# Kernel tuning notes

Hardware: AMD Instinct MI355X
Metric: run time of the kernel (lower is better)

## Reference

```python
import jax, jax.numpy as jnp
import numpy as np
import math

D_MODEL = 1024
N_HEADS = 16
D_HEAD = D_MODEL // N_HEADS

def setup_inputs() -> dict:
    key = jax.random.key(0)
    k1, k2, k3 = jax.random.split(key, 3)
    x = jax.random.normal(k1, (4, 2048, D_MODEL), dtype=jnp.float32)
    # torch Linear weights are [out, in]; kept in that layout, applied as x @ W.T
    s = 1.0 / math.sqrt(D_MODEL)
    W_qkv = jax.random.uniform(k2, (3 * D_MODEL, D_MODEL), jnp.float32, -s, s)
    W_proj = jax.random.uniform(k3, (D_MODEL, D_MODEL), jnp.float32, -s, s)
    return {"x": x, "W_qkv": W_qkv, "W_proj": W_proj}

def reference(x, W_qkv, W_proj):
    B, T, d = x.shape
    qkv = x @ W_qkv.T  # [B,T,3d]
    q, k, v = jnp.split(qkv, 3, axis=-1)
    def split(t):
        return t.reshape(B, T, N_HEADS, D_HEAD).transpose(0, 2, 1, 3)  # [B,H,T,Dh]
    q, k, v = split(q), split(k), split(v)
    scores = jnp.einsum('bhqd,bhkd->bhqk', q, k) / math.sqrt(D_HEAD)
    mask = jnp.tril(jnp.ones((T, T), dtype=bool))
    scores = jnp.where(mask, scores, -jnp.inf)
    attn = jax.nn.softmax(scores, axis=-1)
    out = jnp.einsum('bhqk,bhkd->bhqd', attn, v)  # [B,H,T,Dh]
    out = out.transpose(0, 2, 1, 3).reshape(B, T, d)
    return out @ W_proj.T
```

## Files before the change

kernel.cpp:

```cpp
#include <hip/hip_runtime.h>
#include <hip/hip_bf16.h>
#include <math.h>

typedef __attribute__((ext_vector_type(8))) short short8;
typedef __attribute__((ext_vector_type(4))) float f32x4;
typedef __attribute__((ext_vector_type(16))) float f32x16;
typedef __attribute__((ext_vector_type(2))) unsigned uint2v;
typedef __attribute__((ext_vector_type(4))) unsigned uint4v;

#define B_  4
#define T_  2048
#define DM  1024
#define NH  16
#define DH  64
#define BH  (B_*NH)
#define M_  (B_*T_)

#define QSCALE 0.18033688011112042f

static __device__ __forceinline__ short f2bf(float f) {
  unsigned u = __float_as_uint(f);
  unsigned r = (u + 0x7fff + ((u >> 16) & 1)) >> 16;
  return (short)r;
}

static __device__ __forceinline__ unsigned cvtpk(float lo, float hi) {
  unsigned r;
  asm("v_cvt_pk_bf16_f32 %0, %1, %2" : "=v"(r) : "v"(lo), "v"(hi));
  return r;
}

static __device__ __forceinline__ float expasm(float x) {
  float r;
  asm("v_exp_f32 %0, %1" : "=v"(r) : "v"(x));
  return r;
}

static __device__ __forceinline__ void gload_lds16(const void* g, void* l) {
  __builtin_amdgcn_global_load_lds((const __attribute__((address_space(1))) void*)g,
                                   (__attribute__((address_space(3))) void*)l, 16, 0, 0);
}

__global__ void k_cvt3(const float4* __restrict__ x, const float4* __restrict__ wq,
                       const float4* __restrict__ wp, ushort4* __restrict__ ox,
                       ushort4* __restrict__ oq, ushort4* __restrict__ op) {
  const int n1 = M_ * DM / 4, n2 = 3 * DM * DM / 4, n3 = DM * DM / 4;
  int i = blockIdx.x * 256 + threadIdx.x;
  const float4* src;
  ushort4* dst;
  int j = i;
  if (i < n1) { src = x; dst = ox; }
  else if (i < n1 + n2) { src = wq; dst = oq; j = i - n1; }
  else if (i < n1 + n2 + n3) { src = wp; dst = op; j = i - n1 - n2; }
  else return;
  float4 v = src[j];
  ushort4 o;
  o.x = (ushort)f2bf(v.x); o.y = (ushort)f2bf(v.y);
  o.z = (ushort)f2bf(v.z); o.w = (ushort)f2bf(v.w);
  dst[j] = o;
}

#define GEMM_STAGE(SRCA, SRCB, dA, dB, m0_, n0_, k0_)                          \
  {                                                                            \
    _Pragma("unroll")                                                          \
    for (int i = 0; i < 4; ++i) {                                              \
      int lin = i * 256 + tid;                                                 \
      int row = lin >> 3, pseg = lin & 7;                                      \
      int gseg = pseg ^ (row & 7);                                             \
      gload_lds16(&SRCA[(size_t)((m0_) + row) * DM + (k0_) + gseg * 8],        \
                  &(dA)[lin * 8]);                                             \
    }                                                                          \
    _Pragma("unroll")                                                          \
    for (int i = 0; i < 4; ++i) {                                              \
      int lin = i * 256 + tid;                                                 \
      int row = lin >> 3, pseg = lin & 7;                                      \
      int gseg = pseg ^ (row & 7);                                             \
      gload_lds16(&SRCB[(size_t)((n0_) + row) * DM + (k0_) + gseg * 8],        \
                  &(dB)[lin * 8]);                                             \
    }                                                                          \
  }

#define GEMM_COMPUTE(pA, pB)                                                   \
  {                                                                            \
    _Pragma("unroll")                                                          \
    for (int kk = 0; kk < 2; ++kk) {                                           \
      short8 aF[4], bF[4];                                                     \
      _Pragma("unroll")                                                        \
      for (int m = 0; m < 4; ++m)                                              \
        aF[m] = *(const short8*)&(pA)[(wr * 64 + m * 16 + fr) * 64 +           \
                                      (((kk * 4 + fq) ^ (fr & 7)) * 8)];       \
      _Pragma("unroll")                                                        \
      for (int n = 0; n < 4; ++n)                                              \
        bF[n] = *(const short8*)&(pB)[(wc * 64 + n * 16 + fr) * 64 +           \
                                      (((kk * 4 + fq) ^ (fr & 7)) * 8)];       \
      __builtin_amdgcn_s_setprio(1);                                           \
      _Pragma("unroll")                                                        \
      for (int m = 0; m < 4; ++m)                                              \
        _Pragma("unroll")                                                      \
        for (int n = 0; n < 4; ++n)                                            \
          acc[m][n] = __builtin_amdgcn_mfma_f32_16x16x32_bf16(aF[m], bF[n],    \
                                                              acc[m][n], 0, 0, 0); \
      __builtin_amdgcn_s_setprio(0);                                           \
    }                                                                          \
  }

#define GEMM_KLOOP(SRCA, SRCB, m0_, n0_)                                       \
  GEMM_STAGE(SRCA, SRCB, sA0, sB0, m0_, n0_, 0);                               \
  {                                                                            \
    _Pragma("unroll 1")                                                        \
    for (int t = 0; t < 16; ++t) {                                             \
      short* pA = (t & 1) ? sA1 : sA0;                                         \
      short* pB = (t & 1) ? sB1 : sB0;                                         \
      if (t < 15) {                                                            \
        short* nA = (t & 1) ? sA0 : sA1;                                       \
        short* nB = (t & 1) ? sB0 : sB1;                                       \
        GEMM_STAGE(SRCA, SRCB, nA, nB, m0_, n0_, (t + 1) * 64);                \
        asm volatile("s_waitcnt vmcnt(8)" ::: "memory");                       \
      } else {                                                                 \
        asm volatile("s_waitcnt vmcnt(0)" ::: "memory");                       \
      }                                                                        \
      __builtin_amdgcn_s_barrier();                                            \
      __builtin_amdgcn_sched_barrier(0);                                       \
      GEMM_COMPUTE(pA, pB);                                                    \
      asm volatile("" ::: "memory");                                           \
      __builtin_amdgcn_s_barrier();                                            \
    }                                                                          \
  }

__global__ __launch_bounds__(256, 2) void k_gemm_qkv(
    const short* __restrict__ A,
    const short* __restrict__ W,
    short* __restrict__ Qb, short* __restrict__ Kb, short* __restrict__ Vtb) {
  const int tid = threadIdx.x;
  const int w = tid >> 6, l = tid & 63;
  const int wr = w >> 1, wc = w & 1;
  const int fq = l >> 4, fr = l & 15;
  const int m0 = blockIdx.x * 128;
  const int n0 = blockIdx.y * 128;

  __shared__ short lds[32768];
  short* sA0 = lds;
  short* sA1 = lds + 8192;
  short* sB0 = lds + 16384;
  short* sB1 = lds + 24576;

  f32x4 acc[4][4] = {};
  GEMM_KLOOP(A, W, m0, n0);
  __syncthreads();

  short* sE = lds;
  const int part = n0 >> 10;
  const int b = m0 >> 11, tloc = m0 & 2047;

  if (part < 2) {
    const float sc = part ? 1.0f : QSCALE;
#pragma unroll
    for (int m = 0; m < 4; ++m)
#pragma unroll
      for (int n = 0; n < 4; ++n)
#pragma unroll
        for (int j = 0; j < 4; ++j)
          sE[(wr * 64 + m * 16 + fq * 4 + j) * 136 + wc * 64 + n * 16 + fr] =
              f2bf(acc[m][n][j] * sc);
    __syncthreads();
    short* dst = part ? Kb : Qb;
    const int h0 = (n0 & 1023) >> 6;
#pragma unroll
    for (int v = 0; v < 8; ++v) {
      int vid = v * 256 + tid;
      int row = vid >> 4, seg = vid & 15;
      short8 val = *(const short8*)&sE[row * 136 + seg * 8];
      int h = h0 + (seg >> 3), dh0 = (seg & 7) * 8;
      *(short8*)&dst[(((size_t)(b * NH + h) * T_ + tloc + row)) * DH + dh0] = val;
    }
  } else {
#pragma unroll
    for (int m = 0; m < 4; ++m)
#pragma unroll
      for (int n = 0; n < 4; ++n) {
        uint2v pk;
        pk[0] = cvtpk(acc[m][n][0], acc[m][n][1]);
        pk[1] = cvtpk(acc[m][n][2], acc[m][n][3]);
        *(uint2v*)&sE[(wc * 64 + n * 16 + fr) * 136 + wr * 64 + m * 16 + fq * 4] = pk;
      }
    __syncthreads();
    const int h0 = (n0 & 1023) >> 6;
#pragma unroll
    for (int v = 0; v < 8; ++v) {
      int vid = v * 256 + tid;
      int col = vid >> 4, seg = vid & 15;
      short8 val = *(const short8*)&sE[col * 136 + seg * 8];
      int h = h0 + (col >> 6), dh = col & 63;
      *(short8*)&Vtb[(((size_t)(b * NH + h) * DH + dh)) * T_ + tloc + seg * 8] = val;
    }
  }
}

__global__ __launch_bounds__(256, 2) void k_gemm_proj(
    const short* __restrict__ A,
    const short* __restrict__ W,
    float* __restrict__ C) {
  const int tid = threadIdx.x;
  const int w = tid >> 6, l = tid & 63;
  const int wr = w >> 1, wc = w & 1;
  const int fq = l >> 4, fr = l & 15;
  const int m0 = blockIdx.x * 128;
  const int n0 = blockIdx.y * 128;

  __shared__ short lds[32768];
  short* sA0 = lds;
  short* sA1 = lds + 8192;
  short* sB0 = lds + 16384;
  short* sB1 = lds + 24576;

  f32x4 acc[4][4] = {};
  GEMM_KLOOP(A, W, m0, n0);

#pragma unroll
  for (int m = 0; m < 4; ++m) {
    int row0 = m0 + wr * 64 + m * 16 + fq * 4;
#pragma unroll
    for (int n = 0; n < 4; ++n) {
      int col = n0 + wc * 64 + n * 16 + fr;
#pragma unroll
      for (int j = 0; j < 4; ++j)
        C[(size_t)(row0 + j) * DM + col] = acc[m][n][j];
    }
  }
}

__global__ __launch_bounds__(256, 2) void k_attn7(
    const short* __restrict__ Qb,
    const short* __restrict__ Kb,
    const short* __restrict__ Vtb,
    short* __restrict__ Ob) {
  const int tid = threadIdx.x;
  const int w = tid >> 6, l = tid & 63;
  const int lq = l & 31, hi = l >> 5;
  const int id = blockIdx.x;
  const int u = id >> 6;
  const int bh = id & 63;
  const int qt = (u < 4) ? (7 - u) : (u - 4);
  const int b = bh >> 4, h = bh & 15;

  __shared__ short lds[16384];
  short* sK = lds;
  short* sVt = lds + 8192;

  auto STAGE = [&](int buf, int kt) {
#pragma unroll
    for (int i = 0; i < 2; ++i) {
      int lin = i * 256 + tid;
      int row = lin >> 3, pseg = lin & 7;
      int gseg = pseg ^ (row & 7);
      gload_lds16(&Kb[((size_t)bh * T_ + kt * 64 + row) * DH + gseg * 8],
                  &sK[buf * 4096 + lin * 8]);
    }
#pragma unroll
    for (int i = 0; i < 2; ++i) {
      int lin = i * 256 + tid;
      int row = lin >> 3, pseg = lin & 7;
      int gseg = pseg ^ (row & 7);
      gload_lds16(&Vtb[((size_t)bh * DH + row) * T_ + kt * 64 + gseg * 8],
                  &sVt[buf * 4096 + lin * 8]);
    }
  };

  const int nkt = 4 * qt + 4;
  const int q00 = qt * 256 + w * 32;
  const int q01 = q00 + 128;

  short8 qf0[4], qf1[4];
#pragma unroll
  for (int c = 0; c < 4; ++c) {
    qf0[c] = *(const short8*)&Qb[((size_t)bh * T_ + q00 + lq) * DH + c * 16 + hi * 8];
    qf1[c] = *(const short8*)&Qb[((size_t)bh * T_ + q01 + lq) * DH + c * 16 + hi * 8];
  }
  asm volatile("s_waitcnt vmcnt(0)" ::: "memory");

  float ls0 = 0.f, ls1 = 0.f;
  f32x16 oa0[2] = {}, oa1[2] = {};

  auto CSUB = [&](int kt, const int koff, const short8 (&qf)[4],
                  f32x16 (&oacc)[2], float& lsum, int q0s) {
    f32x16 a0 = {}, a1 = {};
    __builtin_amdgcn_s_setprio(1);
#pragma unroll
    for (int c = 0; c < 4; ++c) {
      short8 kf0 = *(const short8*)&sK[koff + (lq) * 64 + (((2 * c + hi) ^ (lq & 7)) * 8)];
      short8 kf1 = *(const short8*)&sK[koff + (32 + lq) * 64 + (((2 * c + hi) ^ (lq & 7)) * 8)];
      a0 = __builtin_amdgcn_mfma_f32_32x32x16_bf16(kf0, qf[c], a0, 0, 0, 0);
      a1 = __builtin_amdgcn_mfma_f32_32x32x16_bf16(kf1, qf[c], a1, 0, 0, 0);
    }
    __builtin_amdgcn_s_setprio(0);

    if (kt * 64 + 63 > q0s) {
      const int qg = q0s + lq;
#pragma unroll
      for (int r = 0; r < 16; ++r) {
        int kg0 = kt * 64 + (r & 3) + 8 * (r >> 2) + 4 * hi;
        if (kg0 > qg) a0[r] = -1e30f;
        if (kg0 + 32 > qg) a1[r] = -1e30f;
      }
    }

#pragma unroll
    for (int r = 0; r < 16; ++r) {
      a0[r] = expasm(a0[r]);
      a1[r] = expasm(a1[r]);
    }
    {
      float t[8];
#pragma unroll
      for (int i = 0; i < 8; ++i)
        t[i] = (a0[2 * i] + a0[2 * i + 1]) + (a1[2 * i] + a1[2 * i + 1]);
      float u0 = (t[0] + t[1]) + (t[2] + t[3]);
      float u1 = (t[4] + t[5]) + (t[6] + t[7]);
      lsum += u0 + u1;
    }

    short8 pb[4];
#pragma unroll
    for (int st = 0; st < 2; ++st) {
      const f32x16& P = st ? a1 : a0;
      unsigned x0 = cvtpk(P[0], P[1]);
      unsigned x1 = cvtpk(P[2], P[3]);
      unsigned y0 = cvtpk(P[4], P[5]);
      unsigned y1 = cvtpk(P[6], P[7]);
      uint2v r0 = __builtin_amdgcn_permlane32_swap(x0, y0, false, false);
      uint2v r1 = __builtin_amdgcn_permlane32_swap(x1, y1, false, false);
      unsigned x2 = cvtpk(P[8], P[9]);
      unsigned x3 = cvtpk(P[10], P[11]);
      unsigned y2 = cvtpk(P[12], P[13]);
      unsigned y3 = cvtpk(P[14], P[15]);
      uint2v r2 = __builtin_amdgcn_permlane32_swap(x2, y2, false, false);
      uint2v r3 = __builtin_amdgcn_permlane32_swap(x3, y3, false, false);
      uint4v ta, tb;
      ta[0] = r0[0]; ta[1] = r1[0]; ta[2] = r0[1]; ta[3] = r1[1];
      tb[0] = r2[0]; tb[1] = r3[0]; tb[2] = r2[1]; tb[3] = r3[1];
      pb[st * 2 + 0] = __builtin_bit_cast(short8, ta);
      pb[st * 2 + 1] = __builtin_bit_cast(short8, tb);
    }

    __builtin_amdgcn_s_setprio(1);
#pragma unroll
    for (int dt = 0; dt < 2; ++dt) {
#pragma unroll
      for (int c = 0; c < 4; ++c) {
        short8 vf = *(const short8*)&sVt[koff + (dt * 32 + lq) * 64 +
                                         (((2 * c + hi) ^ (lq & 7)) * 8)];
        oacc[dt] = __builtin_amdgcn_mfma_f32_32x32x16_bf16(vf, pb[c], oacc[dt], 0, 0, 0);
      }
    }
    __builtin_amdgcn_s_setprio(0);
  };

  STAGE(0, 0);
  int t = 0;
  while (true) {
    if (t + 1 < nkt) {
      STAGE(1, t + 1);
      asm volatile("s_waitcnt vmcnt(4)" ::: "memory");
    } else {
      asm volatile("s_waitcnt vmcnt(0)" ::: "memory");
    }
    __builtin_amdgcn_s_barrier();
    __builtin_amdgcn_sched_barrier(0);
    if (t * 64 <= q00 + 31) CSUB(t, 0, qf0, oa0, ls0, q00);
    if (t * 64 <= q01 + 31) CSUB(t, 0, qf1, oa1, ls1, q01);
    __builtin_amdgcn_s_barrier();
    if (++t == nkt) break;

    if (t + 1 < nkt) {
      STAGE(0, t + 1);
      asm volatile("s_waitcnt vmcnt(4)" ::: "memory");
    } else {
      asm volatile("s_waitcnt vmcnt(0)" ::: "memory");
    }
    __builtin_amdgcn_s_barrier();
    __builtin_amdgcn_sched_barrier(0);
    if (t * 64 <= q00 + 31) CSUB(t, 4096, qf0, oa0, ls0, q00);
    if (t * 64 <= q01 + 31) CSUB(t, 4096, qf1, oa1, ls1, q01);
    __builtin_amdgcn_s_barrier();
    if (++t == nkt) break;
  }

  ls0 += __shfl_xor(ls0, 32);
  ls1 += __shfl_xor(ls1, 32);
  __syncthreads();
  short* sO = lds + w * 2304;
  const int qr = l >> 1, hf = l & 1;

  {
    float inv = 1.0f / ls0;
#pragma unroll
    for (int dt = 0; dt < 2; ++dt)
#pragma unroll
      for (int r = 0; r < 16; r += 2) {
        int dl = dt * 32 + (r & 3) + 8 * (r >> 2) + 4 * hi;
        *(unsigned*)&sO[lq * 72 + dl] = cvtpk(oa0[dt][r] * inv, oa0[dt][r + 1] * inv);
      }
    asm volatile("s_waitcnt lgkmcnt(0)" ::: "memory");
    __builtin_amdgcn_sched_barrier(0);
    const int tg = q00 - w * 32 + w * 32 + qr;
#pragma unroll
    for (int ss = 0; ss < 4; ++ss) {
      short8 v = *(const short8*)&sO[qr * 72 + hf * 32 + ss * 8];
      *(short8*)&Ob[((size_t)(b * T_) + tg) * DM + h * 64 + hf * 32 + ss * 8] = v;
    }
    asm volatile("s_waitcnt lgkmcnt(0)" ::: "memory");
    __builtin_amdgcn_sched_barrier(0);
  }
  {
    float inv = 1.0f / ls1;
#pragma unroll
    for (int dt = 0; dt < 2; ++dt)
#pragma unroll
      for (int r = 0; r < 16; r += 2) {
        int dl = dt * 32 + (r & 3) + 8 * (r >> 2) + 4 * hi;
        *(unsigned*)&sO[lq * 72 + dl] = cvtpk(oa1[dt][r] * inv, oa1[dt][r + 1] * inv);
      }
    asm volatile("s_waitcnt lgkmcnt(0)" ::: "memory");
    __builtin_amdgcn_sched_barrier(0);
    const int tg = q01 - w * 32 + w * 32 + qr;
#pragma unroll
    for (int ss = 0; ss < 4; ++ss) {
      short8 v = *(const short8*)&sO[qr * 72 + hf * 32 + ss * 8];
      *(short8*)&Ob[((size_t)(b * T_) + tg) * DM + h * 64 + hf * 32 + ss * 8] = v;
    }
  }
}

extern "C" void kernel_launch(void* const* d_in, const int* in_sizes, int n_in,
                              void* d_out, int out_size, void* d_ws, size_t ws_size,
                              hipStream_t stream) {
  const float* x     = (const float*)d_in[0];
  const float* Wqkv  = (const float*)d_in[1];
  const float* Wproj = (const float*)d_in[2];
  float* out = (float*)d_out;

  short* ws = (short*)d_ws;
  short* xbf   = ws;
  short* wqkvb = xbf + (size_t)M_ * DM;
  short* wprjb = wqkvb + (size_t)3 * DM * DM;
  short* Qb    = wprjb + (size_t)DM * DM;
  short* Kb    = Qb + (size_t)BH * T_ * DH;
  short* Vtb   = Kb + (size_t)BH * T_ * DH;
  short* Ob    = Vtb + (size_t)BH * T_ * DH;

  const int ncv = (M_ * DM + 3 * DM * DM + DM * DM) / 4;
  k_cvt3<<<(ncv + 255) / 256, 256, 0, stream>>>(
      (const float4*)x, (const float4*)Wqkv, (const float4*)Wproj,
      (ushort4*)xbf, (ushort4*)wqkvb, (ushort4*)wprjb);

  k_gemm_qkv<<<dim3(M_ / 128, 3 * DM / 128), 256, 0, stream>>>(xbf, wqkvb, Qb, Kb, Vtb);
  k_attn7<<<512, 256, 0, stream>>>(Qb, Kb, Vtb, Ob);
  k_gemm_proj<<<dim3(M_ / 128, DM / 128), 256, 0, stream>>>(Ob, wprjb, out);
}
```

Measured before the change: 141.4 us.

## Split long causal attention tiles across two blocks with a merge kernel

Splits the KV range of the four longest query tiles into two segments: one block takes keys 0-17, and a second block takes the remainder plus one short query tile. Each split writes unnormalized bf16 partial outputs and row sums to scratch that reuses the x/W_qkv bf16 buffers, and a new merge kernel combines them. The aim is to even out per-block work under the causal mask and shorten the tail of the attention launch. The cost is an extra kernel launch, extra global traffic, and bf16 rounding of the partial sums. Adding the partials without max rescaling is only correct because the softmax here is computed without a running max.

```diff
diff --git a/kernel.cpp b/kernel.cpp
--- a/kernel.cpp
+++ b/kernel.cpp
@@ -22,6 +22,10 @@
   unsigned u = __float_as_uint(f);
   unsigned r = (u + 0x7fff + ((u >> 16) & 1)) >> 16;
   return (short)r;
+}
+
+static __device__ __forceinline__ float bf2f(short s) {
+  return __uint_as_float(((unsigned)(unsigned short)s) << 16);
 }
 
 static __device__ __forceinline__ unsigned cvtpk(float lo, float hi) {
@@ -229,18 +233,21 @@
   }
 }
 
-__global__ __launch_bounds__(256, 2) void k_attn7(
+__global__ __launch_bounds__(256, 2) void k_attn8(
     const short* __restrict__ Qb,
     const short* __restrict__ Kb,
     const short* __restrict__ Vtb,
-    short* __restrict__ Ob) {
+    short* __restrict__ Ob,
+    unsigned* __restrict__ Pbuf,
+    float* __restrict__ Lbuf) {
   const int tid = threadIdx.x;
   const int w = tid >> 6, l = tid & 63;
   const int lq = l & 31, hi = l >> 5;
   const int id = blockIdx.x;
-  const int u = id >> 6;
+  const int x = id >> 6;
+  const int u = (x < 4) ? (2 * x) : (2 * (x - 4) + 1);
   const int bh = id & 63;
-  const int qt = (u < 4) ? (7 - u) : (u - 4);
+  const int qtA = 7 - (u >> 1);
   const int b = bh >> 4, h = bh & 15;
 
   __shared__ short lds[16384];
@@ -265,21 +272,6 @@
                   &sVt[buf * 4096 + lin * 8]);
     }
   };
-
-  const int nkt = 4 * qt + 4;
-  const int q00 = qt * 256 + w * 32;
-  const int q01 = q00 + 128;
-
-  short8 qf0[4], qf1[4];
-#pragma unroll
-  for (int c = 0; c < 4; ++c) {
-    qf0[c] = *(const short8*)&Qb[((size_t)bh * T_ + q00 + lq) * DH + c * 16 + hi * 8];
-    qf1[c] = *(const short8*)&Qb[((size_t)bh * T_ + q01 + lq) * DH + c * 16 + hi * 8];
-  }
-  asm volatile("s_waitcnt vmcnt(0)" ::: "memory");
-
-  float ls0 = 0.f, ls1 = 0.f;
-  f32x16 oa0[2] = {}, oa1[2] = {};
 
   auto CSUB = [&](int kt, const int koff, const short8 (&qf)[4],
                   f32x16 (&oacc)[2], float& lsum, int q0s) {
@@ -355,54 +347,159 @@
     __builtin_amdgcn_s_setprio(0);
   };
 
-  STAGE(0, 0);
-  int t = 0;
-  while (true) {
-    if (t + 1 < nkt) {
-      STAGE(1, t + 1);
-      asm volatile("s_waitcnt vmcnt(4)" ::: "memory");
+  auto RUN_SEG = [&](int qt, int k0, int k1, int ppid) {
+    const int q00 = qt * 256 + w * 32;
+    const int q01 = q00 + 128;
+    short8 qf0[4], qf1[4];
+#pragma unroll
+    for (int c = 0; c < 4; ++c) {
+      qf0[c] = *(const short8*)&Qb[((size_t)bh * T_ + q00 + lq) * DH + c * 16 + hi * 8];
+      qf1[c] = *(const short8*)&Qb[((size_t)bh * T_ + q01 + lq) * DH + c * 16 + hi * 8];
+    }
+    float ls0 = 0.f, ls1 = 0.f;
+    f32x16 oa0[2] = {}, oa1[2] = {};
+
+    STAGE(0, k0);
+    int t = k0;
+    while (true) {
+      if (t + 1 < k1) {
+        STAGE(1, t + 1);
+        asm volatile("s_waitcnt vmcnt(4)" ::: "memory");
+      } else {
+        asm volatile("s_waitcnt vmcnt(0)" ::: "memory");
+      }
+      __builtin_amdgcn_s_barrier();
+      __builtin_amdgcn_sched_barrier(0);
+      if (t * 64 <= q00 + 31) CSUB(t, 0, qf0, oa0, ls0, q00);
+      if (t * 64 <= q01 + 31) CSUB(t, 0, qf1, oa1, ls1, q01);
+      __builtin_amdgcn_s_barrier();
+      if (++t == k1) break;
+
+      if (t + 1 < k1) {
+        STAGE(0, t + 1);
+        asm volatile("s_waitcnt vmcnt(4)" ::: "memory");
+      } else {
+        asm volatile("s_waitcnt vmcnt(0)" ::: "memory");
+      }
+      __builtin_amdgcn_s_barrier();
+      __builtin_amdgcn_sched_barrier(0);
+      if (t * 64 <= q00 + 31) CSUB(t, 4096, qf0, oa0, ls0, q00);
+      if (t * 64 <= q01 + 31) CSUB(t, 4096, qf1, oa1, ls1, q01);
+      __builtin_amdgcn_s_barrier();
+      if (++t == k1) break;
+    }
+
+    ls0 += __shfl_xor(ls0, 32);
+    ls1 += __shfl_xor(ls1, 32);
+
+    if (ppid >= 0) {
+      unsigned* Pb = Pbuf + (size_t)ppid * 8192;
+#pragma unroll
+      for (int sub = 0; sub < 2; ++sub) {
+        const f32x16* OA = sub ? oa1 : oa0;
+#pragma unroll
+        for (int dt = 0; dt < 2; ++dt)
+#pragma unroll
+          for (int p = 0; p < 8; ++p)
+            Pb[(((sub * 4 + w) * 2 + dt) * 8 + p) * 64 + l] =
+                cvtpk(OA[dt][2 * p], OA[dt][2 * p + 1]);
+      }
+      if (hi == 0) {
+        Lbuf[ppid * 256 + (0 * 4 + w) * 32 + lq] = ls0;
+        Lbuf[ppid * 256 + (1 * 4 + w) * 32 + lq] = ls1;
+      }
     } else {
-      asm volatile("s_waitcnt vmcnt(0)" ::: "memory");
-    }
-    __builtin_amdgcn_s_barrier();
-    __builtin_amdgcn_sched_barrier(0);
-    if (t * 64 <= q00 + 31) CSUB(t, 0, qf0, oa0, ls0, q00);
-    if (t * 64 <= q01 + 31) CSUB(t, 0, qf1, oa1, ls1, q01);
-    __builtin_amdgcn_s_barrier();
-    if (++t == nkt) break;
-
-    if (t + 1 < nkt) {
-      STAGE(0, t + 1);
-      asm volatile("s_waitcnt vmcnt(4)" ::: "memory");
-    } else {
-      asm volatile("s_waitcnt vmcnt(0)" ::: "memory");
-    }
-    __builtin_amdgcn_s_barrier();
-    __builtin_amdgcn_sched_barrier(0);
-    if (t * 64 <= q00 + 31) CSUB(t, 4096, qf0, oa0, ls0, q00);
-    if (t * 64 <= q01 + 31) CSUB(t, 4096, qf1, oa1, ls1, q01);
-    __builtin_amdgcn_s_barrier();
-    if (++t == nkt) break;
-  }
-
-  ls0 += __shfl_xor(ls0, 32);
-  ls1 += __shfl_xor(ls1, 32);
-  __syncthreads();
-  short* sO = lds + w * 2304;
+      __syncthreads();
+      short* sO = lds + w * 2304;
+      const int qr = l >> 1, hf = l & 1;
+      {
+        float inv = 1.0f / ls0;
+#pragma unroll
+        for (int dt = 0; dt < 2; ++dt)
+#pragma unroll
+          for (int r = 0; r < 16; r += 2) {
+            int dl = dt * 32 + (r & 3) + 8 * (r >> 2) + 4 * hi;
+            *(unsigned*)&sO[lq * 72 + dl] = cvtpk(oa0[dt][r] * inv, oa0[dt][r + 1] * inv);
+          }
+        asm volatile("s_waitcnt lgkmcnt(0)" ::: "memory");
+        __builtin_amdgcn_sched_barrier(0);
+        const int tg = qt * 256 + w * 32 + qr;
+#pragma unroll
+        for (int ss = 0; ss < 4; ++ss) {
+          short8 v = *(const short8*)&sO[qr * 72 + hf * 32 + ss * 8];
+          *(short8*)&Ob[((size_t)(b * T_) + tg) * DM + h * 64 + hf * 32 + ss * 8] = v;
+        }
+        asm volatile("s_waitcnt lgkmcnt(0)" ::: "memory");
+        __builtin_amdgcn_sched_barrier(0);
+      }
+      {
+        float inv = 1.0f / ls1;
+#pragma unroll
+        for (int dt = 0; dt < 2; ++dt)
+#pragma unroll
+          for (int r = 0; r < 16; r += 2) {
+            int dl = dt * 32 + (r & 3) + 8 * (r >> 2) + 4 * hi;
+            *(unsigned*)&sO[lq * 72 + dl] = cvtpk(oa1[dt][r] * inv, oa1[dt][r + 1] * inv);
+          }
+        asm volatile("s_waitcnt lgkmcnt(0)" ::: "memory");
+        __builtin_amdgcn_sched_barrier(0);
+        const int tg = qt * 256 + 128 + w * 32 + qr;
+#pragma unroll
+        for (int ss = 0; ss < 4; ++ss) {
+          short8 v = *(const short8*)&sO[qr * 72 + hf * 32 + ss * 8];
+          *(short8*)&Ob[((size_t)(b * T_) + tg) * DM + h * 64 + hf * 32 + ss * 8] = v;
+        }
+      }
+    }
+  };
+
+  if ((u & 1) == 0) {
+    RUN_SEG(qtA, 0, 18, (bh * 4 + (qtA - 4)) * 2 + 0);
+  } else {
+    RUN_SEG(qtA, 18, 4 * qtA + 4, (bh * 4 + (qtA - 4)) * 2 + 1);
+    const int qtB = u >> 1;
+    RUN_SEG(qtB, 0, 4 * qtB + 4, -1);
+  }
+}
+
+__global__ __launch_bounds__(256) void k_merge(
+    const unsigned* __restrict__ P, const float* __restrict__ L,
+    short* __restrict__ Ob) {
+  const int tid = threadIdx.x;
+  const int w = tid >> 6, l = tid & 63;
+  const int lq = l & 31, hi = l >> 5;
+  const int sid = blockIdx.x;
+  const int bh = sid & 63, qtm = sid >> 6;
+  const int qt = 4 + qtm;
+  const int b = bh >> 4, h = bh & 15;
+  const int pid0 = (bh * 4 + qtm) * 2;
+  const unsigned* P0 = P + (size_t)pid0 * 8192;
+  const unsigned* P1 = P0 + 8192;
+
+  __shared__ short sOm[9216];
+  short* sO = sOm + w * 2304;
   const int qr = l >> 1, hf = l & 1;
 
-  {
-    float inv = 1.0f / ls0;
+#pragma unroll
+  for (int sub = 0; sub < 2; ++sub) {
+    float l0 = L[pid0 * 256 + (sub * 4 + w) * 32 + lq];
+    float l1 = L[(pid0 + 1) * 256 + (sub * 4 + w) * 32 + lq];
+    float inv = 1.0f / (l0 + l1);
 #pragma unroll
     for (int dt = 0; dt < 2; ++dt)
 #pragma unroll
-      for (int r = 0; r < 16; r += 2) {
+      for (int p = 0; p < 8; ++p) {
+        int idx = (((sub * 4 + w) * 2 + dt) * 8 + p) * 64 + l;
+        unsigned u0 = P0[idx], u1 = P1[idx];
+        float e0 = bf2f((short)(u0 & 0xffff)) + bf2f((short)(u1 & 0xffff));
+        float e1 = bf2f((short)(u0 >> 16)) + bf2f((short)(u1 >> 16));
+        int r = 2 * p;
         int dl = dt * 32 + (r & 3) + 8 * (r >> 2) + 4 * hi;
-        *(unsigned*)&sO[lq * 72 + dl] = cvtpk(oa0[dt][r] * inv, oa0[dt][r + 1] * inv);
+        *(unsigned*)&sO[lq * 72 + dl] = cvtpk(e0 * inv, e1 * inv);
       }
     asm volatile("s_waitcnt lgkmcnt(0)" ::: "memory");
     __builtin_amdgcn_sched_barrier(0);
-    const int tg = q00 - w * 32 + w * 32 + qr;
+    const int tg = qt * 256 + sub * 128 + w * 32 + qr;
 #pragma unroll
     for (int ss = 0; ss < 4; ++ss) {
       short8 v = *(const short8*)&sO[qr * 72 + hf * 32 + ss * 8];
@@ -410,24 +507,6 @@
     }
     asm volatile("s_waitcnt lgkmcnt(0)" ::: "memory");
     __builtin_amdgcn_sched_barrier(0);
-  }
-  {
-    float inv = 1.0f / ls1;
-#pragma unroll
-    for (int dt = 0; dt < 2; ++dt)
-#pragma unroll
-      for (int r = 0; r < 16; r += 2) {
-        int dl = dt * 32 + (r & 3) + 8 * (r >> 2) + 4 * hi;
-        *(unsigned*)&sO[lq * 72 + dl] = cvtpk(oa1[dt][r] * inv, oa1[dt][r + 1] * inv);
-      }
-    asm volatile("s_waitcnt lgkmcnt(0)" ::: "memory");
-    __builtin_amdgcn_sched_barrier(0);
-    const int tg = q01 - w * 32 + w * 32 + qr;
-#pragma unroll
-    for (int ss = 0; ss < 4; ++ss) {
-      short8 v = *(const short8*)&sO[qr * 72 + hf * 32 + ss * 8];
-      *(short8*)&Ob[((size_t)(b * T_) + tg) * DM + h * 64 + hf * 32 + ss * 8] = v;
-    }
   }
 }
 
@@ -447,6 +526,8 @@
   short* Kb    = Qb + (size_t)BH * T_ * DH;
   short* Vtb   = Kb + (size_t)BH * T_ * DH;
   short* Ob    = Vtb + (size_t)BH * T_ * DH;
+  unsigned* Pbuf = (unsigned*)xbf;
+  float* Lbuf    = (float*)wqkvb;
 
   const int ncv = (M_ * DM + 3 * DM * DM + DM * DM) / 4;
   k_cvt3<<<(ncv + 255) / 256, 256, 0, stream>>>(
@@ -454,6 +535,7 @@
       (ushort4*)xbf, (ushort4*)wqkvb, (ushort4*)wprjb);
 
   k_gemm_qkv<<<dim3(M_ / 128, 3 * DM / 128), 256, 0, stream>>>(xbf, wqkvb, Qb, Kb, Vtb);
-  k_attn7<<<512, 256, 0, stream>>>(Qb, Kb, Vtb, Ob);
+  k_attn8<<<512, 256, 0, stream>>>(Qb, Kb, Vtb, Ob, Pbuf, Lbuf);
+  k_merge<<<256, 256, 0, stream>>>(Pbuf, Lbuf, Ob);
   k_gemm_proj<<<dim3(M_ / 128, DM / 128), 256, 0, stream>>>(Ob, wprjb, out);
 }
```

New measurement: 142.6 us. No clear change (+0.8%).
